# Kernel optimization log

Hardware: AMD Instinct MI355X
Metric: run time of the kernel (lower is better)

Reference implementation:

```python
import jax, jax.numpy as jnp
import numpy as np

ROT = 0.7071  # matches the literal used in DiagPool's affine theta
EPS = 1e-5    # GroupNorm default eps


def conv2d(x, w, pad):
    # x: (N,C,H,W), w: (O,I,kh,kw)
    return jax.lax.conv_general_dilated(
        x, w, window_strides=(1, 1), padding=[(pad, pad), (pad, pad)],
        dimension_numbers=("NCHW", "OIHW", "NCHW"))


def diag_pool(x):
    """Replicates F.affine_grid + F.grid_sample (align_corners=False, bilinear,
    zeros padding) with a 45-degree rotation, then mean over H (keepdim)."""
    N, C, H, W = x.shape
    dt = x.dtype
    xn = ((2.0 * jnp.arange(W, dtype=dt) + 1.0) / W - 1.0)  # normalized x coords
    yn = ((2.0 * jnp.arange(H, dtype=dt) + 1.0) / H - 1.0)  # normalized y coords
    Yn, Xn = jnp.meshgrid(yn, xn, indexing="ij")            # (H,W)
    xs = ROT * Xn - ROT * Yn   # theta row 0
    ys = ROT * Xn + ROT * Yn   # theta row 1
    # unnormalize (align_corners=False)
    xp = ((xs + 1.0) * W - 1.0) * 0.5
    yp = ((ys + 1.0) * H - 1.0) * 0.5
    x0 = jnp.floor(xp); y0 = jnp.floor(yp)
    x1 = x0 + 1.0;      y1 = y0 + 1.0
    wx1 = xp - x0; wx0 = 1.0 - wx1
    wy1 = yp - y0; wy0 = 1.0 - wy1

    def gather(yi, xi):
        valid = ((yi >= 0) & (yi < H) & (xi >= 0) & (xi < W)).astype(dt)
        yc = jnp.clip(yi, 0, H - 1).astype(jnp.int32)
        xc = jnp.clip(xi, 0, W - 1).astype(jnp.int32)
        return x[:, :, yc, xc] * valid  # (N,C,H,W)

    rot = (gather(y0, x0) * (wy0 * wx0) + gather(y0, x1) * (wy0 * wx1)
           + gather(y1, x0) * (wy1 * wx0) + gather(y1, x1) * (wy1 * wx1))
    return rot.mean(axis=2, keepdims=True)  # (N,C,1,W)


def group_norm_per_channel(x, g, b):
    # GroupNorm(cg, cg): each channel normalized over its own (H,W)
    mu = x.mean(axis=(2, 3), keepdims=True)
    var = x.var(axis=(2, 3), keepdims=True)
    xh = (x - mu) * jax.lax.rsqrt(var + EPS)
    return xh * g[None, :, None, None] + b[None, :, None, None]


def cross_axis_encode(gx, axis_fuse_w, gn_w, gn_b):
    N, cg, H, W = gx.shape
    x_h = gx.mean(axis=3, keepdims=True)                 # (N,cg,H,1)
    x_w = gx.mean(axis=2, keepdims=True)                 # (N,cg,1,W)
    x_d = diag_pool(gx)                                  # (N,cg,1,W)
    fused = jnp.concatenate(
        [x_h, x_w.transpose(0, 1, 3, 2), x_d.transpose(0, 1, 3, 2)], axis=2)  # (N,cg,H+2W,1)
    fused = conv2d(fused, axis_fuse_w, 0)
    x_h2 = fused[:, :, :H]          # (N,cg,H,1)
    x_w2 = fused[:, :, H:H + W]     # (N,cg,W,1)
    out = gx * jax.nn.sigmoid(x_h2) * jax.nn.sigmoid(x_w2.transpose(0, 1, 3, 2))
    return group_norm_per_channel(out, gn_w, gn_b)


def setup_inputs() -> dict:
    key = jax.random.key(0)
    B, C, H, W = 8, 256, 128, 128
    G = 32
    cg = C // G  # 8
    ks = jax.random.split(key, 10)
    s = 0.1
    return {
        "x": jax.random.normal(ks[0], (B, C, H, W), jnp.float32),
        "axis_fuse_w": jax.random.normal(ks[1], (cg, cg, 1, 1), jnp.float32) * s,
        "gn_w": jnp.ones((cg,), jnp.float32),
        "gn_b": jnp.zeros((cg,), jnp.float32),
        "conv1x1_w": jax.random.normal(ks[2], (cg, cg, 1, 1), jnp.float32) * s,
        "conv3x3_w": jax.random.normal(ks[3], (cg, cg, 3, 3), jnp.float32) * s,
        "conv5x5_w": jax.random.normal(ks[4], (cg, cg, 5, 5), jnp.float32) * s,
        "scale_w": jnp.ones((3,), jnp.float32),
        "ch_gate_w": jax.random.normal(ks[5], (cg, cg, 1, 1), jnp.float32) * s,
        "sp_gate_w": jax.random.normal(ks[6], (1, cg, 1, 1), jnp.float32) * s,
        "groups": 32,
    }


def reference(x, axis_fuse_w, gn_w, gn_b, conv1x1_w, conv3x3_w, conv5x5_w,
              scale_w, ch_gate_w, sp_gate_w, groups):
    B, C, H, W = x.shape
    cg = C // groups
    N = B * groups
    gx = x.reshape(N, cg, H, W)

    xa = cross_axis_encode(gx, axis_fuse_w, gn_w, gn_b)
    xa = conv2d(xa, conv1x1_w, 0)
    xb = conv2d(gx, conv3x3_w, 1)
    xc = conv2d(gx, conv5x5_w, 2)

    sw = jax.nn.softmax(scale_w)
    x1 = sw[0] * xa + sw[1] * xb + sw[2] * xc
    x2 = xb

    def ch_gate(t):
        return jax.nn.sigmoid(conv2d(t.mean(axis=(2, 3), keepdims=True), ch_gate_w, 0))

    def sp_gate(t):
        return jax.nn.sigmoid(conv2d(t, sp_gate_w, 0))

    x1 = x1 * ch_gate(x1) * sp_gate(x1)
    x2 = x2 * ch_gate(x2) * sp_gate(x2)

    x11 = jax.nn.softmax(x1.mean(axis=(2, 3)).reshape(N, 1, cg), axis=-1)  # (N,1,cg)
    x12 = x2.reshape(N, cg, H * W)
    x21 = jax.nn.softmax(x2.mean(axis=(2, 3)).reshape(N, 1, cg), axis=-1)
    x22 = x1.reshape(N, cg, H * W)
    weights = (x11 @ x12 + x21 @ x22).reshape(N, 1, H, W)
    return (gx * jax.nn.sigmoid(weights)).reshape(B, C, H, W)
```

## Files before the change

kernel.cpp:

```cpp
#include <hip/hip_runtime.h>
#include <math.h>

#define HH 128
#define WW 128
#define CG 8
#define NN 256
#define HWSZ (HH*WW)

typedef __bf16 bf16x8 __attribute__((ext_vector_type(8)));
typedef short short8v __attribute__((ext_vector_type(8)));
typedef float f32x4 __attribute__((ext_vector_type(4)));

__device__ __forceinline__ float sigmoidf_(float x){ return 1.0f/(1.0f+__expf(-x)); }

__device__ __forceinline__ unsigned short f2bf(float x){
  __bf16 h = (__bf16)x;
  return __builtin_bit_cast(unsigned short, h);
}
__device__ __forceinline__ float bf2f(unsigned short h){
  union { unsigned u; float f; } v; v.u = ((unsigned)h) << 16; return v.f;
}

__global__ void kW(const float* __restrict__ w5, const float* __restrict__ scw,
                   float* __restrict__ w5s){
  int i = blockIdx.x*256 + threadIdx.x;
  if (i >= CG*CG*25) return;
  float a = scw[0], b = scw[1], c = scw[2];
  float m = fmaxf(a, fmaxf(b, c));
  float e0 = __expf(a-m), e1 = __expf(b-m), e2 = __expf(c-m);
  float sw2 = e2 / (e0+e1+e2);
  w5s[i] = sw2 * w5[i];
}

__global__ __launch_bounds__(256) void kA1(const float* __restrict__ gx,
                                           float* __restrict__ xh_ws,
                                           float* __restrict__ xw_ws){
  int b = blockIdx.x; int n = b >> 3; int c = b & 7;
  int tid = threadIdx.x;
  __shared__ float colpart[2][WW];
  const float* img = gx + (size_t)(n*CG+c)*HWSZ;
  int w = tid & 127, half = tid >> 7;
  float acc = 0.f;
  const float* p = img + half*64*WW + w;
  for (int h = 0; h < 64; ++h) acc += p[h*WW];
  colpart[half][w] = acc;
  int h2 = tid >> 1, wh = tid & 1;
  float racc = 0.f;
  const float* rp = img + h2*WW + wh*64;
  for (int j = 0; j < 64; ++j) racc += rp[j];
  racc += __shfl_xor(racc, 1);
  __syncthreads();
  if (tid < WW) xw_ws[(n*CG+c)*WW + tid] = (colpart[0][tid] + colpart[1][tid]) * (1.0f/HH);
  if (wh == 0) xh_ws[(n*CG+c)*HH + h2] = racc * (1.0f/WW);
}

__global__ __launch_bounds__(256) void kA2(const float* __restrict__ xh_ws,
                                           const float* __restrict__ xw_ws,
                                           const float* __restrict__ afw,
                                           float* __restrict__ sig_h,
                                           float* __restrict__ sig_w){
  int n = blockIdx.x;
  int tid = threadIdx.x;
  if (tid < HH){
    int h = tid;
    float v[CG];
    #pragma unroll
    for (int c = 0; c < CG; ++c) v[c] = xh_ws[(n*CG+c)*HH + h];
    #pragma unroll
    for (int o = 0; o < CG; ++o){
      float s = 0.f;
      #pragma unroll
      for (int i = 0; i < CG; ++i) s = fmaf(afw[o*CG+i], v[i], s);
      sig_h[(n*CG+o)*HH + h] = sigmoidf_(s);
    }
  } else {
    int w = tid - 128;
    float v[CG];
    #pragma unroll
    for (int c = 0; c < CG; ++c) v[c] = xw_ws[(n*CG+c)*WW + w];
    #pragma unroll
    for (int o = 0; o < CG; ++o){
      float s = 0.f;
      #pragma unroll
      for (int i = 0; i < CG; ++i) s = fmaf(afw[o*CG+i], v[i], s);
      sig_w[(n*CG+o)*WW + w] = sigmoidf_(s);
    }
  }
}

__global__ __launch_bounds__(256) void kB(const float* __restrict__ gx,
                                          const float* __restrict__ sig_h,
                                          const float* __restrict__ sig_w,
                                          const float* __restrict__ gn_w,
                                          const float* __restrict__ gn_b,
                                          float* __restrict__ Agn,
                                          float* __restrict__ Bgn){
  int b = blockIdx.x; int n = b >> 3; int c = b & 7;
  int tid = threadIdx.x;
  __shared__ float sh[HH];
  __shared__ float swv[WW];
  __shared__ float red[16];
  if (tid < HH) sh[tid] = sig_h[(n*CG+c)*HH + tid];
  else          swv[tid-128] = sig_w[(n*CG+c)*WW + tid - 128];
  __syncthreads();
  const float* img = gx + (size_t)(n*CG+c)*HWSZ;
  float s1 = 0.f, s2 = 0.f;
  for (int idx = tid; idx < HWSZ; idx += 256){
    int h = idx >> 7, w = idx & 127;
    float t = img[idx] * sh[h] * swv[w];
    s1 += t; s2 = fmaf(t, t, s2);
  }
  #pragma unroll
  for (int off = 32; off; off >>= 1){ s1 += __shfl_down(s1, off); s2 += __shfl_down(s2, off); }
  int wv = tid >> 6, ln = tid & 63;
  if (ln == 0){ red[wv] = s1; red[8+wv] = s2; }
  __syncthreads();
  if (tid == 0){
    float S1 = red[0]+red[1]+red[2]+red[3];
    float S2 = red[8]+red[9]+red[10]+red[11];
    float mu  = S1 * (1.0f/HWSZ);
    float var = S2 * (1.0f/HWSZ) - mu*mu;
    float rstd = rsqrtf(var + 1e-5f);
    float A = rstd * gn_w[c];
    Agn[n*CG+c] = A;
    Bgn[n*CG+c] = gn_b[c] - mu*A;
  }
}

__global__ __launch_bounds__(256) void kC(const float* __restrict__ gx,
                                          const float* __restrict__ w1,
                                          const float* __restrict__ w3,
                                          const float* __restrict__ w5s,
                                          const float* __restrict__ scale_w,
                                          const float* __restrict__ spw,
                                          const float* __restrict__ sig_h,
                                          const float* __restrict__ sig_w,
                                          const float* __restrict__ Agn,
                                          const float* __restrict__ Bgn,
                                          unsigned short* __restrict__ x1m,
                                          unsigned short* __restrict__ x2m,
                                          float* __restrict__ gacc){
  __shared__ __align__(16) unsigned short tile[68*36*8];
  __shared__ __align__(16) unsigned short Bm[7][16][32];
  __shared__ __align__(16) unsigned short BmLo[7][10][32];
  __shared__ float sighs[CG][32];
  __shared__ float sigws[CG][32];
  __shared__ float constA[CG];
  __shared__ float wred[4][32];

  int tid = threadIdx.x;
  int bb = blockIdx.x;
  int n  = bb >> 4;
  int t_ = bb & 15;
  int y0 = (t_ >> 2) * 32;
  int x0 = (t_ & 3) * 32;

  float sw0, sw1;
  {
    float a = scale_w[0], b = scale_w[1], c = scale_w[2];
    float m = fmaxf(a, fmaxf(b, c));
    float e0 = __expf(a-m), e1 = __expf(b-m), e2 = __expf(c-m);
    float inv = 1.0f/(e0+e1+e2);
    sw0 = e0*inv; sw1 = e1*inv;
  }
  {
    int ic = tid >> 5, k = tid & 31;
    sighs[ic][k] = sig_h[(n*CG+ic)*HH + y0 + k];
    sigws[ic][k] = sig_w[(n*CG+ic)*WW + x0 + k];
  }
  if (tid < CG){
    float s = 0.f;
    #pragma unroll
    for (int i = 0; i < CG; ++i) s = fmaf(w1[tid*CG+i], Bgn[n*CG+i], s);
    constA[tid] = sw0 * s;
  }

  const float* base_n = gx + (size_t)n*CG*HWSZ;
  for (int e = tid; e < 1296; e += 256){
    int yy = e / 36, xx = e - yy*36;
    int gy = y0 + yy - 2, gz = x0 + xx - 2;
    uint4 pk;
    unsigned* pw = (unsigned*)&pk;
    if ((unsigned)gy < HH && (unsigned)gz < WW){
      int o = gy*WW + gz;
      #pragma unroll
      for (int p = 0; p < 4; ++p){
        float v0 = base_n[(size_t)(2*p)*HWSZ + o];
        float v1 = base_n[(size_t)(2*p+1)*HWSZ + o];
        pw[p] = (unsigned)f2bf(v0) | ((unsigned)f2bf(v1) << 16);
      }
    } else {
      pw[0] = pw[1] = pw[2] = pw[3] = 0u;
    }
    *reinterpret_cast<uint4*>(&tile[e*8]) = pk;
  }

  for (int e = tid; e < 3584; e += 256){
    int s   = e >> 9;
    int rem = e & 511;
    int nn = rem >> 5, kk = rem & 31;
    int tap = s*4 + (kk >> 3);
    int ic  = kk & 7;
    int ky = tap/5, kx = tap - ky*5;
    bool in3 = (tap < 25) && (ky >= 1) && (ky <= 3) && (kx >= 1) && (kx <= 3);
    float wv = 0.f;
    if (nn < 8){
      if (tap < 25){
        wv = w5s[nn*200 + ic*25 + tap];
        if (in3) wv = fmaf(sw1, w3[nn*72 + ic*9 + (ky-1)*3 + (kx-1)], wv);
      } else if (tap == 25){
        wv = sw0 * w1[nn*CG + ic] * Agn[n*CG + ic];
      }
      unsigned short hi = f2bf(wv);
      Bm[s][nn][kk]   = hi;
      BmLo[s][nn][kk] = f2bf(wv - bf2f(hi));
    } else {
      if (in3) wv = w3[(nn-8)*72 + ic*9 + (ky-1)*3 + (kx-1)];
      Bm[s][nn][kk] = f2bf(wv);
    }
  }
  for (int e = tid; e < 448; e += 256){
    int s   = e >> 6;
    int rem = e & 63;
    int col = rem >> 5;
    int kk  = rem & 31;
    int tap = s*4 + (kk >> 3);
    int ic  = kk & 7;
    int ky = tap/5, kx = tap - ky*5;
    bool in3 = (tap < 25) && (ky >= 1) && (ky <= 3) && (kx >= 1) && (kx <= 3);
    float sum = 0.f;
    #pragma unroll
    for (int oc = 0; oc < 8; ++oc){
      float wv = 0.f;
      if (col == 0){
        if (tap < 25){
          wv = w5s[oc*200 + ic*25 + tap];
          if (in3) wv = fmaf(sw1, w3[oc*72 + ic*9 + (ky-1)*3 + (kx-1)], wv);
        } else if (tap == 25){
          wv = sw0 * w1[oc*CG + ic] * Agn[n*CG + ic];
        }
      } else {
        if (in3) wv = w3[oc*72 + ic*9 + (ky-1)*3 + (kx-1)];
      }
      sum = fmaf(spw[oc], wv, sum);
    }
    BmLo[s][8+col][kk] = f2bf(sum);
  }
  __syncthreads();

  for (int e = tid; e < 1024; e += 256){
    int yl = e >> 5, xl = e & 31;
    uint4 pk = *reinterpret_cast<const uint4*>(&tile[((yl+2)*36 + (xl+2))*8]);
    unsigned* pw = (unsigned*)&pk;
    #pragma unroll
    for (int p = 0; p < 4; ++p){
      float g0 = sighs[2*p][yl]   * sigws[2*p][xl];
      float g1 = sighs[2*p+1][yl] * sigws[2*p+1][xl];
      float v0 = bf2f((unsigned short)(pw[p] & 0xffffu)) * g0;
      float v1 = bf2f((unsigned short)(pw[p] >> 16))     * g1;
      pw[p] = (unsigned)f2bf(v0) | ((unsigned)f2bf(v1) << 16);
    }
    *reinterpret_cast<uint4*>(&tile[((yl+36)*36 + (xl+2))*8]) = pk;
  }

  int lane = tid & 63;
  int wid  = tid >> 6;
  int pr = lane & 15;
  int tg = lane >> 4;
  short8v zs = {0,0,0,0,0,0,0,0};
  bf16x8 zb = __builtin_bit_cast(bf16x8, zs);
  bf16x8 bH[7], bL[7];
  int ofs[7];
  #pragma unroll
  for (int s = 0; s < 7; ++s){
    bH[s] = *reinterpret_cast<const bf16x8*>(&Bm[s][pr][tg*8]);
    bL[s] = (pr < 10) ? *reinterpret_cast<const bf16x8*>(&BmLo[s][pr][tg*8]) : zb;
    int t = s*4 + tg;
    int ky, kx;
    if (t < 25){ ky = t/5; kx = t - ky*5; }
    else if (t == 25){ ky = 36; kx = 2; }
    else { ky = 0; kx = 0; }
    ofs[s] = (ky*36 + kx)*8;
  }
  float Cd1 = 0.f;
  #pragma unroll
  for (int oc = 0; oc < CG; ++oc) Cd1 = fmaf(spw[oc], constA[oc], Cd1);
  __syncthreads();

  float cA   = (pr < 8) ? constA[pr] : 0.f;
  int  gsrc  = (lane & 48) | (pr < 8 ? 8 : 9);
  float sAcc = 0.f, qAcc = 0.f;

  #pragma unroll 2
  for (int i = 0; i < 16; ++i){
    int mb = wid*16 + i;
    int yl = mb >> 1;
    int xh = (mb & 1) << 4;
    const unsigned short* abase = &tile[(yl*36 + xh + pr)*8];
    f32x4 accP = {0.f,0.f,0.f,0.f};
    f32x4 accQ = {0.f,0.f,0.f,0.f};
    #pragma unroll
    for (int s = 0; s < 7; ++s){
      bf16x8 a = *reinterpret_cast<const bf16x8*>(abase + ofs[s]);
      accP = __builtin_amdgcn_mfma_f32_16x16x32_bf16(a, bH[s], accP, 0, 0, 0);
      accQ = __builtin_amdgcn_mfma_f32_16x16x32_bf16(a, bL[s], accQ, 0, 0, 0);
    }
    float gq[4];
    #pragma unroll
    for (int r = 0; r < 4; ++r) gq[r] = __shfl(accQ[r], gsrc);
    ushort4 u;
    #pragma unroll
    for (int r = 0; r < 4; ++r){
      float vvr = (pr < 8) ? (accP[r] + accQ[r] + cA) : accP[r];
      float d   = (pr < 8) ? (gq[r] + Cd1) : gq[r];
      float sg  = sigmoidf_(d);
      sAcc += vvr;
      qAcc = fmaf(vvr, sg, qAcc);
      ((unsigned short*)&u)[r] = f2bf(vvr);
    }
    int gy  = y0 + yl;
    int gxx = x0 + xh + tg*4;
    size_t off = ((size_t)(n*CG + (pr & 7))*HH + gy)*WW + gxx;
    if (pr < 8) *reinterpret_cast<ushort4*>(x1m + off) = u;
    else        *reinterpret_cast<ushort4*>(x2m + off) = u;
  }

  sAcc += __shfl_xor(sAcc, 16); sAcc += __shfl_xor(sAcc, 32);
  qAcc += __shfl_xor(qAcc, 16); qAcc += __shfl_xor(qAcc, 32);
  if (lane < 16){
    int b0 = (pr < 8) ? pr : (8 + pr);
    wred[wid][b0]     = sAcc;
    wred[wid][b0 + 8] = qAcc;
  }
  __syncthreads();
  if (tid < 32){
    float s = wred[0][tid] + wred[1][tid] + wred[2][tid] + wred[3][tid];
    atomicAdd(&gacc[n*32 + tid], s);
  }
}

__global__ void kT(const float* __restrict__ gacc, const float* __restrict__ cgw,
                   float* __restrict__ a1a2){
  int n = blockIdx.x*blockDim.x + threadIdx.x;
  if (n >= NN) return;
  const float* g = gacc + n*32;
  float m1[CG], q1[CG], m2[CG], q2[CG];
  #pragma unroll
  for (int c = 0; c < CG; ++c){
    m1[c] = g[c]      * (1.0f/HWSZ);
    q1[c] = g[8+c]    * (1.0f/HWSZ);
    m2[c] = g[16+c]   * (1.0f/HWSZ);
    q2[c] = g[24+c]   * (1.0f/HWSZ);
  }
  float chg1[CG], chg2[CG];
  #pragma unroll
  for (int o = 0; o < CG; ++o){
    float s1 = 0.f, s2 = 0.f;
    #pragma unroll
    for (int i = 0; i < CG; ++i){ s1 = fmaf(cgw[o*CG+i], m1[i], s1); s2 = fmaf(cgw[o*CG+i], m2[i], s2); }
    chg1[o] = sigmoidf_(s1); chg2[o] = sigmoidf_(s2);
  }
  float z1[CG], z2[CG];
  float mx1 = -1e30f, mx2 = -1e30f;
  #pragma unroll
  for (int c = 0; c < CG; ++c){
    z1[c] = chg1[c]*q1[c]; z2[c] = chg2[c]*q2[c];
    mx1 = fmaxf(mx1, z1[c]); mx2 = fmaxf(mx2, z2[c]);
  }
  float su1 = 0.f, su2 = 0.f;
  #pragma unroll
  for (int c = 0; c < CG; ++c){
    z1[c] = __expf(z1[c]-mx1); su1 += z1[c];
    z2[c] = __expf(z2[c]-mx2); su2 += z2[c];
  }
  float i1 = 1.0f/su1, i2 = 1.0f/su2;
  #pragma unroll
  for (int c = 0; c < CG; ++c){
    float x11 = z1[c]*i1;
    float x21 = z2[c]*i2;
    a1a2[n*16 + c]     = x21 * chg1[c];
    a1a2[n*16 + 8 + c] = x11 * chg2[c];
  }
}

__global__ __launch_bounds__(256) void kF(const float* __restrict__ gx,
                                          const unsigned short* __restrict__ x1m,
                                          const unsigned short* __restrict__ x2m,
                                          const float* __restrict__ a1a2,
                                          const float* __restrict__ spw,
                                          float* __restrict__ out){
  int tid = threadIdx.x;
  int bb = blockIdx.x;
  int n  = bb >> 4;
  int hw = ((bb & 15) << 10) + tid*4;
  size_t base = (size_t)(n*CG)*HWSZ + hw;
  float a1[CG], a2[CG], sp[CG];
  #pragma unroll
  for (int c = 0; c < CG; ++c){
    a1[c] = a1a2[n*16 + c];
    a2[c] = a1a2[n*16 + 8 + c];
    sp[c] = spw[c];
  }
  float d1[4]  = {0.f,0.f,0.f,0.f}, dd1[4] = {0.f,0.f,0.f,0.f};
  float d2[4]  = {0.f,0.f,0.f,0.f}, dd2[4] = {0.f,0.f,0.f,0.f};
  #pragma unroll
  for (int c = 0; c < CG; ++c){
    ushort4 u1 = *reinterpret_cast<const ushort4*>(x1m + base + (size_t)c*HWSZ);
    ushort4 u2 = *reinterpret_cast<const ushort4*>(x2m + base + (size_t)c*HWSZ);
    #pragma unroll
    for (int p = 0; p < 4; ++p){
      float v1 = bf2f(((const unsigned short*)&u1)[p]);
      float v2 = bf2f(((const unsigned short*)&u2)[p]);
      d1[p]  = fmaf(sp[c], v1, d1[p]);  dd1[p] = fmaf(a1[c], v1, dd1[p]);
      d2[p]  = fmaf(sp[c], v2, d2[p]);  dd2[p] = fmaf(a2[c], v2, dd2[p]);
    }
  }
  float sW[4];
  #pragma unroll
  for (int p = 0; p < 4; ++p){
    float Wv = sigmoidf_(d1[p])*dd1[p] + sigmoidf_(d2[p])*dd2[p];
    sW[p] = sigmoidf_(Wv);
  }
  #pragma unroll
  for (int c = 0; c < CG; ++c){
    float4 g = *reinterpret_cast<const float4*>(gx + base + (size_t)c*HWSZ);
    float4 o;
    o.x = g.x*sW[0]; o.y = g.y*sW[1]; o.z = g.z*sW[2]; o.w = g.w*sW[3];
    *reinterpret_cast<float4*>(out + base + (size_t)c*HWSZ) = o;
  }
}

extern "C" void kernel_launch(void* const* d_in, const int* in_sizes, int n_in,
                              void* d_out, int out_size, void* d_ws, size_t ws_size,
                              hipStream_t stream){
  const float* x   = (const float*)d_in[0];
  const float* afw = (const float*)d_in[1];
  const float* gnw = (const float*)d_in[2];
  const float* gnb = (const float*)d_in[3];
  const float* w1  = (const float*)d_in[4];
  const float* w3  = (const float*)d_in[5];
  const float* w5  = (const float*)d_in[6];
  const float* scw = (const float*)d_in[7];
  const float* cgw = (const float*)d_in[8];
  const float* spw = (const float*)d_in[9];

  char* ws = (char*)d_ws;
  float* sig_h = (float*)(ws + 0);
  float* sig_w = (float*)(ws + 1048576);
  float* Agn   = (float*)(ws + 2097152);
  float* Bgn   = (float*)(ws + 2105344);
  float* gacc  = (float*)(ws + 2113536);
  float* a1a2  = (float*)(ws + 2146304);
  float* w5s   = (float*)(ws + 2146304);
  unsigned short* x1m = (unsigned short*)(ws + 2162688);
  unsigned short* x2m = (unsigned short*)(ws + 2162688 + 67108864);
  float* out = (float*)d_out;
  float* xh_ws = (float*)d_out;
  float* xw_ws = (float*)d_out + 262144;

  hipMemsetAsync(gacc, 0, NN*32*sizeof(float), stream);
  kW <<<7, 256, 0, stream>>>(w5, scw, w5s);
  kA1<<<NN*CG, 256, 0, stream>>>(x, xh_ws, xw_ws);
  kA2<<<NN, 256, 0, stream>>>(xh_ws, xw_ws, afw, sig_h, sig_w);
  kB <<<NN*CG, 256, 0, stream>>>(x, sig_h, sig_w, gnw, gnb, Agn, Bgn);
  kC <<<NN*16, 256, 0, stream>>>(x, w1, w3, w5s, scw, spw, sig_h, sig_w, Agn, Bgn, x1m, x2m, gacc);
  kT <<<4, 64, 0, stream>>>(gacc, cgw, a1a2);
  kF <<<NN*16, 256, 0, stream>>>(x, x1m, x2m, a1a2, spw, out);
}
```

Measured before the change: 486.6 us.

## Precompute MFMA weight matrices once and fold GroupNorm scale into row gate

Moves construction of the bf16 hi/lo MFMA weight matrices out of every kC block into a single tiny kernel kWB, which works because the GroupNorm scale is now folded into the per-row sigmoid gate (sighA) written by kB. kC loads the B fragments straight from global memory. It builds the gated tile directly from the fp32 values while loading, which saves an LDS pass and one sync. Each wave now processes two 16-pixel blocks per row with interleaved MFMAs and issues atomics per wave rather than through a shared reduction. The cost is more global atomics and extra workspace placed inside the output buffer.

```diff
diff --git a/kernel.cpp b/kernel.cpp
--- a/kernel.cpp
+++ b/kernel.cpp
@@ -6,6 +6,7 @@
 #define CG 8
 #define NN 256
 #define HWSZ (HH*WW)
+#define GB (36*36*8)
 
 typedef __bf16 bf16x8 __attribute__((ext_vector_type(8)));
 typedef short short8v __attribute__((ext_vector_type(8)));
@@ -21,15 +22,64 @@
   union { unsigned u; float f; } v; v.u = ((unsigned)h) << 16; return v.f;
 }
 
-__global__ void kW(const float* __restrict__ w5, const float* __restrict__ scw,
-                   float* __restrict__ w5s){
-  int i = blockIdx.x*256 + threadIdx.x;
-  if (i >= CG*CG*25) return;
+__device__ __forceinline__ float wx1_(const float* w1, const float* w3, const float* w5,
+                                      float sw0, float sw1, float sw2,
+                                      int oc, int ic, int tap){
+  if (tap < 25){
+    int ky = tap/5, kx = tap - ky*5;
+    float wv = sw2 * w5[oc*200 + ic*25 + tap];
+    if (ky >= 1 && ky <= 3 && kx >= 1 && kx <= 3)
+      wv = fmaf(sw1, w3[oc*72 + ic*9 + (ky-1)*3 + (kx-1)], wv);
+    return wv;
+  }
+  if (tap == 25) return sw0 * w1[oc*CG + ic];
+  return 0.f;
+}
+__device__ __forceinline__ float wx2_(const float* w3, int oc, int ic, int tap){
+  if (tap < 25){
+    int ky = tap/5, kx = tap - ky*5;
+    if (ky >= 1 && ky <= 3 && kx >= 1 && kx <= 3)
+      return w3[oc*72 + ic*9 + (ky-1)*3 + (kx-1)];
+  }
+  return 0.f;
+}
+
+__global__ void kWB(const float* __restrict__ w1, const float* __restrict__ w3,
+                    const float* __restrict__ w5, const float* __restrict__ scw,
+                    const float* __restrict__ spw,
+                    unsigned short* __restrict__ BH, unsigned short* __restrict__ BL){
+  int e = blockIdx.x*256 + threadIdx.x;
   float a = scw[0], b = scw[1], c = scw[2];
   float m = fmaxf(a, fmaxf(b, c));
   float e0 = __expf(a-m), e1 = __expf(b-m), e2 = __expf(c-m);
-  float sw2 = e2 / (e0+e1+e2);
-  w5s[i] = sw2 * w5[i];
+  float inv = 1.0f/(e0+e1+e2);
+  float sw0 = e0*inv, sw1 = e1*inv, sw2 = e2*inv;
+  if (e < 3584){
+    int s = e >> 9, rem = e & 511, nn = rem >> 5, kk = rem & 31;
+    int tap = s*4 + (kk >> 3), ic = kk & 7;
+    float wv = (nn < 8) ? wx1_(w1,w3,w5,sw0,sw1,sw2,nn,ic,tap)
+                        : wx2_(w3,nn-8,ic,tap);
+    BH[e] = f2bf(wv);
+  } else if (e < 5824){
+    int e2 = e - 3584;
+    int s = e2 / 320, rem = e2 - s*320, nn = rem >> 5, kk = rem & 31;
+    int tap = s*4 + (kk >> 3), ic = kk & 7;
+    float outv;
+    if (nn < 8){
+      float wv = wx1_(w1,w3,w5,sw0,sw1,sw2,nn,ic,tap);
+      outv = wv - bf2f(f2bf(wv));
+    } else {
+      float sum = 0.f;
+      #pragma unroll
+      for (int oc = 0; oc < CG; ++oc){
+        float wv = (nn == 8) ? wx1_(w1,w3,w5,sw0,sw1,sw2,oc,ic,tap)
+                             : wx2_(w3,oc,ic,tap);
+        sum = fmaf(spw[oc], wv, sum);
+      }
+      outv = sum;
+    }
+    BL[e2] = f2bf(outv);
+  }
 }
 
 __global__ __launch_bounds__(256) void kA1(const float* __restrict__ gx,
@@ -93,13 +143,14 @@
                                           const float* __restrict__ sig_w,
                                           const float* __restrict__ gn_w,
                                           const float* __restrict__ gn_b,
-                                          float* __restrict__ Agn,
-                                          float* __restrict__ Bgn){
+                                          float* __restrict__ Bgn,
+                                          float* __restrict__ sighA){
   int b = blockIdx.x; int n = b >> 3; int c = b & 7;
   int tid = threadIdx.x;
   __shared__ float sh[HH];
   __shared__ float swv[WW];
   __shared__ float red[16];
+  __shared__ float sAb;
   if (tid < HH) sh[tid] = sig_h[(n*CG+c)*HH + tid];
   else          swv[tid-128] = sig_w[(n*CG+c)*WW + tid - 128];
   __syncthreads();
@@ -122,31 +173,29 @@
     float var = S2 * (1.0f/HWSZ) - mu*mu;
     float rstd = rsqrtf(var + 1e-5f);
     float A = rstd * gn_w[c];
-    Agn[n*CG+c] = A;
     Bgn[n*CG+c] = gn_b[c] - mu*A;
-  }
+    sAb = A;
+  }
+  __syncthreads();
+  if (tid < HH) sighA[(n*CG+c)*HH + tid] = sh[tid] * sAb;
 }
 
 __global__ __launch_bounds__(256) void kC(const float* __restrict__ gx,
                                           const float* __restrict__ w1,
-                                          const float* __restrict__ w3,
-                                          const float* __restrict__ w5s,
                                           const float* __restrict__ scale_w,
                                           const float* __restrict__ spw,
-                                          const float* __restrict__ sig_h,
                                           const float* __restrict__ sig_w,
-                                          const float* __restrict__ Agn,
+                                          const float* __restrict__ sighA,
                                           const float* __restrict__ Bgn,
+                                          const unsigned short* __restrict__ BHg,
+                                          const unsigned short* __restrict__ BLog,
                                           unsigned short* __restrict__ x1m,
                                           unsigned short* __restrict__ x2m,
                                           float* __restrict__ gacc){
-  __shared__ __align__(16) unsigned short tile[68*36*8];
-  __shared__ __align__(16) unsigned short Bm[7][16][32];
-  __shared__ __align__(16) unsigned short BmLo[7][10][32];
-  __shared__ float sighs[CG][32];
-  __shared__ float sigws[CG][32];
+  __shared__ __align__(16) unsigned short tile[36*36*8 + 32*32*8];
+  __shared__ float shf[CG*32];
+  __shared__ float swf[CG*32];
   __shared__ float constA[CG];
-  __shared__ float wred[4][32];
 
   int tid = threadIdx.x;
   int bb = blockIdx.x;
@@ -155,18 +204,35 @@
   int y0 = (t_ >> 2) * 32;
   int x0 = (t_ & 3) * 32;
 
-  float sw0, sw1;
+  int lane = tid & 63, wid = tid >> 6;
+  int pr = lane & 15, tg = lane >> 4;
+
+  bf16x8 bH[7], bL[7];
+  #pragma unroll
+  for (int s = 0; s < 7; ++s)
+    bH[s] = *reinterpret_cast<const bf16x8*>(BHg + s*512 + pr*32 + tg*8);
+  short8v zs = {0,0,0,0,0,0,0,0};
+  bf16x8 zb = __builtin_bit_cast(bf16x8, zs);
+  if (pr < 10){
+    #pragma unroll
+    for (int s = 0; s < 7; ++s)
+      bL[s] = *reinterpret_cast<const bf16x8*>(BLog + s*320 + pr*32 + tg*8);
+  } else {
+    #pragma unroll
+    for (int s = 0; s < 7; ++s) bL[s] = zb;
+  }
+
+  float sw0;
   {
     float a = scale_w[0], b = scale_w[1], c = scale_w[2];
     float m = fmaxf(a, fmaxf(b, c));
     float e0 = __expf(a-m), e1 = __expf(b-m), e2 = __expf(c-m);
-    float inv = 1.0f/(e0+e1+e2);
-    sw0 = e0*inv; sw1 = e1*inv;
+    sw0 = e0 / (e0+e1+e2);
   }
   {
     int ic = tid >> 5, k = tid & 31;
-    sighs[ic][k] = sig_h[(n*CG+ic)*HH + y0 + k];
-    sigws[ic][k] = sig_w[(n*CG+ic)*WW + x0 + k];
+    shf[ic*32+k] = sighA[(n*CG+ic)*HH + y0 + k];
+    swf[ic*32+k] = sig_w[(n*CG+ic)*WW + x0 + k];
   }
   if (tid < CG){
     float s = 0.f;
@@ -174,168 +240,102 @@
     for (int i = 0; i < CG; ++i) s = fmaf(w1[tid*CG+i], Bgn[n*CG+i], s);
     constA[tid] = sw0 * s;
   }
+  __syncthreads();
 
   const float* base_n = gx + (size_t)n*CG*HWSZ;
   for (int e = tid; e < 1296; e += 256){
     int yy = e / 36, xx = e - yy*36;
     int gy = y0 + yy - 2, gz = x0 + xx - 2;
-    uint4 pk;
-    unsigned* pw = (unsigned*)&pk;
+    float v[8];
+    uint4 pk; unsigned* pw = (unsigned*)&pk;
     if ((unsigned)gy < HH && (unsigned)gz < WW){
       int o = gy*WW + gz;
       #pragma unroll
       for (int p = 0; p < 4; ++p){
-        float v0 = base_n[(size_t)(2*p)*HWSZ + o];
-        float v1 = base_n[(size_t)(2*p+1)*HWSZ + o];
-        pw[p] = (unsigned)f2bf(v0) | ((unsigned)f2bf(v1) << 16);
+        v[2*p]   = base_n[(size_t)(2*p)*HWSZ + o];
+        v[2*p+1] = base_n[(size_t)(2*p+1)*HWSZ + o];
+        pw[p] = (unsigned)f2bf(v[2*p]) | ((unsigned)f2bf(v[2*p+1]) << 16);
       }
     } else {
-      pw[0] = pw[1] = pw[2] = pw[3] = 0u;
+      #pragma unroll
+      for (int p = 0; p < 4; ++p){ v[2*p] = 0.f; v[2*p+1] = 0.f; pw[p] = 0u; }
     }
     *reinterpret_cast<uint4*>(&tile[e*8]) = pk;
-  }
-
-  for (int e = tid; e < 3584; e += 256){
-    int s   = e >> 9;
-    int rem = e & 511;
-    int nn = rem >> 5, kk = rem & 31;
-    int tap = s*4 + (kk >> 3);
-    int ic  = kk & 7;
-    int ky = tap/5, kx = tap - ky*5;
-    bool in3 = (tap < 25) && (ky >= 1) && (ky <= 3) && (kx >= 1) && (kx <= 3);
-    float wv = 0.f;
-    if (nn < 8){
-      if (tap < 25){
-        wv = w5s[nn*200 + ic*25 + tap];
-        if (in3) wv = fmaf(sw1, w3[nn*72 + ic*9 + (ky-1)*3 + (kx-1)], wv);
-      } else if (tap == 25){
-        wv = sw0 * w1[nn*CG + ic] * Agn[n*CG + ic];
+    int yl = yy - 2, xl = xx - 2;
+    if ((unsigned)yl < 32u && (unsigned)xl < 32u){
+      uint4 gk; unsigned* gw = (unsigned*)&gk;
+      #pragma unroll
+      for (int p = 0; p < 4; ++p){
+        float t0 = v[2*p]   * shf[(2*p)*32   + yl] * swf[(2*p)*32   + xl];
+        float t1 = v[2*p+1] * shf[(2*p+1)*32 + yl] * swf[(2*p+1)*32 + xl];
+        gw[p] = (unsigned)f2bf(t0) | ((unsigned)f2bf(t1) << 16);
       }
-      unsigned short hi = f2bf(wv);
-      Bm[s][nn][kk]   = hi;
-      BmLo[s][nn][kk] = f2bf(wv - bf2f(hi));
-    } else {
-      if (in3) wv = w3[(nn-8)*72 + ic*9 + (ky-1)*3 + (kx-1)];
-      Bm[s][nn][kk] = f2bf(wv);
-    }
-  }
-  for (int e = tid; e < 448; e += 256){
-    int s   = e >> 6;
-    int rem = e & 63;
-    int col = rem >> 5;
-    int kk  = rem & 31;
-    int tap = s*4 + (kk >> 3);
-    int ic  = kk & 7;
-    int ky = tap/5, kx = tap - ky*5;
-    bool in3 = (tap < 25) && (ky >= 1) && (ky <= 3) && (kx >= 1) && (kx <= 3);
-    float sum = 0.f;
-    #pragma unroll
-    for (int oc = 0; oc < 8; ++oc){
-      float wv = 0.f;
-      if (col == 0){
-        if (tap < 25){
-          wv = w5s[oc*200 + ic*25 + tap];
-          if (in3) wv = fmaf(sw1, w3[oc*72 + ic*9 + (ky-1)*3 + (kx-1)], wv);
-        } else if (tap == 25){
-          wv = sw0 * w1[oc*CG + ic] * Agn[n*CG + ic];
-        }
-      } else {
-        if (in3) wv = w3[oc*72 + ic*9 + (ky-1)*3 + (kx-1)];
-      }
-      sum = fmaf(spw[oc], wv, sum);
-    }
-    BmLo[s][8+col][kk] = f2bf(sum);
-  }
-  __syncthreads();
-
-  for (int e = tid; e < 1024; e += 256){
-    int yl = e >> 5, xl = e & 31;
-    uint4 pk = *reinterpret_cast<const uint4*>(&tile[((yl+2)*36 + (xl+2))*8]);
-    unsigned* pw = (unsigned*)&pk;
-    #pragma unroll
-    for (int p = 0; p < 4; ++p){
-      float g0 = sighs[2*p][yl]   * sigws[2*p][xl];
-      float g1 = sighs[2*p+1][yl] * sigws[2*p+1][xl];
-      float v0 = bf2f((unsigned short)(pw[p] & 0xffffu)) * g0;
-      float v1 = bf2f((unsigned short)(pw[p] >> 16))     * g1;
-      pw[p] = (unsigned)f2bf(v0) | ((unsigned)f2bf(v1) << 16);
-    }
-    *reinterpret_cast<uint4*>(&tile[((yl+36)*36 + (xl+2))*8]) = pk;
-  }
-
-  int lane = tid & 63;
-  int wid  = tid >> 6;
-  int pr = lane & 15;
-  int tg = lane >> 4;
-  short8v zs = {0,0,0,0,0,0,0,0};
-  bf16x8 zb = __builtin_bit_cast(bf16x8, zs);
-  bf16x8 bH[7], bL[7];
-  int ofs[7];
+      *reinterpret_cast<uint4*>(&tile[GB + (yl*32 + xl)*8]) = gk;
+    }
+  }
+
+  int strd[7], ofs[7];
   #pragma unroll
   for (int s = 0; s < 7; ++s){
-    bH[s] = *reinterpret_cast<const bf16x8*>(&Bm[s][pr][tg*8]);
-    bL[s] = (pr < 10) ? *reinterpret_cast<const bf16x8*>(&BmLo[s][pr][tg*8]) : zb;
     int t = s*4 + tg;
-    int ky, kx;
-    if (t < 25){ ky = t/5; kx = t - ky*5; }
-    else if (t == 25){ ky = 36; kx = 2; }
-    else { ky = 0; kx = 0; }
-    ofs[s] = (ky*36 + kx)*8;
+    if (t < 25){ int ky = t/5, kx = t - ky*5; strd[s] = 36*8; ofs[s] = (ky*36 + kx)*8; }
+    else if (t == 25){ strd[s] = 32*8; ofs[s] = GB; }
+    else { strd[s] = 36*8; ofs[s] = 0; }
   }
   float Cd1 = 0.f;
   #pragma unroll
   for (int oc = 0; oc < CG; ++oc) Cd1 = fmaf(spw[oc], constA[oc], Cd1);
-  __syncthreads();
-
-  float cA   = (pr < 8) ? constA[pr] : 0.f;
-  int  gsrc  = (lane & 48) | (pr < 8 ? 8 : 9);
+  float cA = (pr < 8) ? constA[pr] : 0.f;
+  int gsrc = (lane & 48) | (pr < 8 ? 8 : 9);
+  __syncthreads();
+
   float sAcc = 0.f, qAcc = 0.f;
 
-  #pragma unroll 2
-  for (int i = 0; i < 16; ++i){
-    int mb = wid*16 + i;
-    int yl = mb >> 1;
-    int xh = (mb & 1) << 4;
-    const unsigned short* abase = &tile[(yl*36 + xh + pr)*8];
-    f32x4 accP = {0.f,0.f,0.f,0.f};
-    f32x4 accQ = {0.f,0.f,0.f,0.f};
+#define EPI(P, Q, GXX) do { \
+    float gq[4]; \
+    _Pragma("unroll") \
+    for (int r = 0; r < 4; ++r) gq[r] = __shfl(Q[r], gsrc); \
+    ushort4 u; \
+    _Pragma("unroll") \
+    for (int r = 0; r < 4; ++r){ \
+      float vvr = (pr < 8) ? (P[r] + Q[r] + cA) : P[r]; \
+      float d   = (pr < 8) ? (gq[r] + Cd1) : gq[r]; \
+      float sg  = sigmoidf_(d); \
+      sAcc += vvr; \
+      qAcc = fmaf(vvr, sg, qAcc); \
+      ((unsigned short*)&u)[r] = f2bf(vvr); \
+    } \
+    size_t off = ((size_t)(n*CG + (pr & 7))*HH + (y0 + yl))*WW + (GXX); \
+    if (pr < 8) *reinterpret_cast<ushort4*>(x1m + off) = u; \
+    else        *reinterpret_cast<ushort4*>(x2m + off) = u; \
+  } while(0)
+
+  #pragma unroll 1
+  for (int ii = 0; ii < 8; ++ii){
+    int yl = wid*8 + ii;
+    f32x4 P0 = {0.f,0.f,0.f,0.f}, Q0 = {0.f,0.f,0.f,0.f};
+    f32x4 P1 = {0.f,0.f,0.f,0.f}, Q1 = {0.f,0.f,0.f,0.f};
     #pragma unroll
     for (int s = 0; s < 7; ++s){
-      bf16x8 a = *reinterpret_cast<const bf16x8*>(abase + ofs[s]);
-      accP = __builtin_amdgcn_mfma_f32_16x16x32_bf16(a, bH[s], accP, 0, 0, 0);
-      accQ = __builtin_amdgcn_mfma_f32_16x16x32_bf16(a, bL[s], accQ, 0, 0, 0);
-    }
-    float gq[4];
-    #pragma unroll
-    for (int r = 0; r < 4; ++r) gq[r] = __shfl(accQ[r], gsrc);
-    ushort4 u;
-    #pragma unroll
-    for (int r = 0; r < 4; ++r){
-      float vvr = (pr < 8) ? (accP[r] + accQ[r] + cA) : accP[r];
-      float d   = (pr < 8) ? (gq[r] + Cd1) : gq[r];
-      float sg  = sigmoidf_(d);
-      sAcc += vvr;
-      qAcc = fmaf(vvr, sg, qAcc);
-      ((unsigned short*)&u)[r] = f2bf(vvr);
-    }
-    int gy  = y0 + yl;
-    int gxx = x0 + xh + tg*4;
-    size_t off = ((size_t)(n*CG + (pr & 7))*HH + gy)*WW + gxx;
-    if (pr < 8) *reinterpret_cast<ushort4*>(x1m + off) = u;
-    else        *reinterpret_cast<ushort4*>(x2m + off) = u;
-  }
+      const unsigned short* ap = &tile[yl*strd[s] + ofs[s] + pr*8];
+      bf16x8 a0 = *reinterpret_cast<const bf16x8*>(ap);
+      bf16x8 a1 = *reinterpret_cast<const bf16x8*>(ap + 128);
+      P0 = __builtin_amdgcn_mfma_f32_16x16x32_bf16(a0, bH[s], P0, 0, 0, 0);
+      Q0 = __builtin_amdgcn_mfma_f32_16x16x32_bf16(a0, bL[s], Q0, 0, 0, 0);
+      P1 = __builtin_amdgcn_mfma_f32_16x16x32_bf16(a1, bH[s], P1, 0, 0, 0);
+      Q1 = __builtin_amdgcn_mfma_f32_16x16x32_bf16(a1, bL[s], Q1, 0, 0, 0);
+    }
+    EPI(P0, Q0, x0 + tg*4);
+    EPI(P1, Q1, x0 + 16 + tg*4);
+  }
+#undef EPI
 
   sAcc += __shfl_xor(sAcc, 16); sAcc += __shfl_xor(sAcc, 32);
   qAcc += __shfl_xor(qAcc, 16); qAcc += __shfl_xor(qAcc, 32);
   if (lane < 16){
     int b0 = (pr < 8) ? pr : (8 + pr);
-    wred[wid][b0]     = sAcc;
-    wred[wid][b0 + 8] = qAcc;
-  }
-  __syncthreads();
-  if (tid < 32){
-    float s = wred[0][tid] + wred[1][tid] + wred[2][tid] + wred[3][tid];
-    atomicAdd(&gacc[n*32 + tid], s);
+    atomicAdd(&gacc[n*32 + b0],     sAcc);
+    atomicAdd(&gacc[n*32 + b0 + 8], qAcc);
   }
 }
 
@@ -447,23 +447,25 @@
   char* ws = (char*)d_ws;
   float* sig_h = (float*)(ws + 0);
   float* sig_w = (float*)(ws + 1048576);
-  float* Agn   = (float*)(ws + 2097152);
-  float* Bgn   = (float*)(ws + 2105344);
-  float* gacc  = (float*)(ws + 2113536);
-  float* a1a2  = (float*)(ws + 2146304);
-  float* w5s   = (float*)(ws + 2146304);
-  unsigned short* x1m = (unsigned short*)(ws + 2162688);
-  unsigned short* x2m = (unsigned short*)(ws + 2162688 + 67108864);
+  unsigned short* BHg  = (unsigned short*)(ws + 2097152);
+  float* a1a2 = (float*)(ws + 2097152);
+  unsigned short* BLog = (unsigned short*)(ws + 2113536);
+  unsigned short* x1m = (unsigned short*)(ws + 2121728);
+  unsigned short* x2m = (unsigned short*)(ws + 2121728 + 67108864);
+
   float* out = (float*)d_out;
   float* xh_ws = (float*)d_out;
   float* xw_ws = (float*)d_out + 262144;
+  float* sighA = (float*)((char*)d_out + 2097152);
+  float* Bgn   = (float*)((char*)d_out + 3145728);
+  float* gacc  = (float*)((char*)d_out + 3153920);
 
   hipMemsetAsync(gacc, 0, NN*32*sizeof(float), stream);
-  kW <<<7, 256, 0, stream>>>(w5, scw, w5s);
+  kWB<<<23, 256, 0, stream>>>(w1, w3, w5, scw, spw, BHg, BLog);
   kA1<<<NN*CG, 256, 0, stream>>>(x, xh_ws, xw_ws);
   kA2<<<NN, 256, 0, stream>>>(xh_ws, xw_ws, afw, sig_h, sig_w);
-  kB <<<NN*CG, 256, 0, stream>>>(x, sig_h, sig_w, gnw, gnb, Agn, Bgn);
-  kC <<<NN*16, 256, 0, stream>>>(x, w1, w3, w5s, scw, spw, sig_h, sig_w, Agn, Bgn, x1m, x2m, gacc);
+  kB <<<NN*CG, 256, 0, stream>>>(x, sig_h, sig_w, gnw, gnb, Bgn, sighA);
+  kC <<<NN*16, 256, 0, stream>>>(x, w1, scw, spw, sig_w, sighA, Bgn, BHg, BLog, x1m, x2m, gacc);
   kT <<<4, 64, 0, stream>>>(gacc, cgw, a1a2);
   kF <<<NN*16, 256, 0, stream>>>(x, x1m, x2m, a1a2, spw, out);
 }
```

Result: faster. 447.1 us (-8.1%).
